# Kernel tuning notes

Hardware: AMD Instinct MI355X
Metric: run time of the kernel (lower is better)

Reference implementation:

```python
import jax, jax.numpy as jnp
import numpy as np

SIGMA = 45.0
N, M, D = 4096, 4096, 1024


def setup_inputs() -> dict:
    key = jax.random.key(0)
    k1, k2 = jax.random.split(key)
    inputs = jax.random.normal(k1, (N, D), dtype=jnp.float32)
    samples = jax.random.normal(k2, (M, D), dtype=jnp.float32)
    return {"inputs": inputs, "samples": samples}


def _sq_dists(x, y):
    # ||x_i||^2 + ||y_j||^2 - 2 x_i.y_j  -> [N, M]
    prod = x @ y.T
    xs = jnp.sum(x * x, axis=1)[:, None]
    ys = jnp.sum(y * y, axis=1)[None, :]
    return xs + ys - 2.0 * prod


def reference(inputs, samples):
    n = inputs.shape[0]
    m = samples.shape[0]
    x = inputs.reshape(n, -1)
    y = samples.reshape(m, -1)
    inv_s2 = 1.0 / (SIGMA ** 2)

    k_xx = _sq_dists(x, x)
    k_yy = _sq_dists(y, y)
    k_xy = _sq_dists(x, y)

    # unbiased MMD: exclude diagonal terms of k_xx, k_yy
    exx = jnp.exp(-k_xx * inv_s2)
    eyy = jnp.exp(-k_yy * inv_s2)
    exy = jnp.exp(-k_xy * inv_s2)

    mmd = (jnp.sum(exx) - jnp.sum(jnp.exp(-jnp.diag(k_xx) * inv_s2))) / (n * (n - 1))
    mmd = mmd + (jnp.sum(eyy) - jnp.sum(jnp.exp(-jnp.diag(k_yy) * inv_s2))) / (m * (m - 1))
    mmd = mmd - 2.0 / (n * m) * jnp.sum(exy)
    return mmd
```

## Files before the change

kernel.cpp:

```cpp
#include <hip/hip_runtime.h>
#include <math.h>


typedef _Float16 f16_t;
typedef _Float16 f16x4 __attribute__((ext_vector_type(4)));
typedef _Float16 f16x8 __attribute__((ext_vector_type(8)));
typedef float floatx4 __attribute__((ext_vector_type(4)));

#define NROWS 4096
#define MROWS 4096
#define DDIM  1024
#define BM    128
#define BK    32
#define TILE  (BM * BK)
#define NKT   (DDIM / BK)
#define PSTRIDE (4096 * BK)
#define NT    (NROWS / BM)
#define TRI   (NT * (NT + 1) / 2)
#define NBLK  (2 * TRI + NT * NT)

__global__ __launch_bounds__(256) void convert_kernel(
    const float* __restrict__ X, const float* __restrict__ Y,
    f16_t* __restrict__ Xp, f16_t* __restrict__ Yp,
    float* __restrict__ nx, float* __restrict__ ny) {
    const int wid  = threadIdx.x >> 6;
    const int lane = threadIdx.x & 63;
    const int row  = blockIdx.x * 4 + wid;
    const float* src;
    f16_t* dstp;
    float* nrm;
    int r;
    if (row < NROWS) {
        r = row;         src = X + (size_t)r * DDIM;
        dstp = Xp;  nrm = nx;
    } else {
        r = row - NROWS; src = Y + (size_t)r * DDIM;
        dstp = Yp;  nrm = ny;
    }
    const float4* s4 = (const float4*)src;
    float s = 0.f;
    #pragma unroll
    for (int c = 0; c < 4; c++) {
        float4 v = s4[c * 64 + lane];
        f16x4 h;
        h[0] = (f16_t)v.x; h[1] = (f16_t)v.y;
        h[2] = (f16_t)v.z; h[3] = (f16_t)v.w;
        *(f16x4*)(dstp + (size_t)(c * 8 + (lane >> 3)) * PSTRIDE
                       + (size_t)r * BK + (lane & 7) * 4) = h;
        float h0 = (float)h[0], h1 = (float)h[1];
        float h2 = (float)h[2], h3 = (float)h[3];
        s += h0 * h0 + h1 * h1 + h2 * h2 + h3 * h3;
    }
    #pragma unroll
    for (int off = 32; off > 0; off >>= 1) s += __shfl_down(s, off);
    if (lane == 0) nrm[r] = s;
}

__global__ __launch_bounds__(256) void mmd_mfma(
    const f16_t* __restrict__ Xp, const f16_t* __restrict__ Yp,
    const float* __restrict__ nx, const float* __restrict__ ny,
    double* __restrict__ partials) {
    __shared__ __align__(16) f16_t ldsA[TILE];
    __shared__ double wred[4];

    const int b = blockIdx.x;
    const f16_t *Ap, *Bp;
    const float *nA, *nB;
    int tr, tc;
    double coef;
    if (b < 2 * TRI) {
        int u = (b < TRI) ? b : b - TRI;
        int r = 0;
        while (u >= NT - r) { u -= NT - r; r++; }
        tr = r; tc = r + u;
        double w = (tr == tc) ? 1.0 : 2.0;
        if (b < TRI) { Ap = Xp; Bp = Xp; nA = nx; nB = nx;
                       coef = w / ((double)NROWS * (double)(NROWS - 1)); }
        else         { Ap = Yp; Bp = Yp; nA = ny; nB = ny;
                       coef = w / ((double)MROWS * (double)(MROWS - 1)); }
    } else {
        int u = b - 2 * TRI;
        tr = u >> 5; tc = u & 31;
        Ap = Xp; Bp = Yp; nA = nx; nB = ny;
        coef = -2.0 / ((double)NROWS * (double)MROWS);
    }

    const int t    = threadIdx.x;
    const int wave = t >> 6;
    const int lane = t & 63;
    const int wm   = wave >> 1;
    const int wn   = wave & 1;

    const int lr = lane >> 2;
    const int lc = (lane & 3) ^ ((lane >> 3) & 3);
    const f16_t* gsrc[2];
    f16_t* ldst[2];
    #pragma unroll
    for (int i = 0; i < 2; i++) {
        int rg = wave * 2 + i;
        gsrc[i] = Ap + (size_t)(tr * BM + rg * 16 + lr) * BK + lc * 8;
        ldst[i] = ldsA + rg * 16 * BK;
    }

    const int m    = lane & 15;
    const int quad = lane >> 4;
    const int sw8  = (quad ^ ((m >> 1) & 3)) * 8;

    const f16_t* gB = Bp + (size_t)(tc * BM + wn * 64 + m) * BK + quad * 8;

    float na[16], nb[4];
    #pragma unroll
    for (int i = 0; i < 4; i++) {
        #pragma unroll
        for (int r = 0; r < 4; r++)
            na[i * 4 + r] = nA[tr * BM + wm * 64 + i * 16 + quad * 4 + r];
        nb[i] = nB[tc * BM + wn * 64 + i * 16 + m];
    }

    floatx4 acc_r[4][4];
    #pragma unroll
    for (int i = 0; i < 4; i++)
        #pragma unroll
        for (int j = 0; j < 4; j++) acc_r[i][j] = (floatx4){0.f, 0.f, 0.f, 0.f};

    for (int kt = 0; kt < NKT; kt++) {
        const size_t ko = (size_t)kt * PSTRIDE;
        __syncthreads();
        #pragma unroll
        for (int i = 0; i < 2; i++) {
            __builtin_amdgcn_global_load_lds(
                (const __attribute__((address_space(1))) void*)(gsrc[i] + ko),
                (__attribute__((address_space(3))) void*)ldst[i],
                16, 0, 0);
        }
        __syncthreads();

        f16x8 bh[4];
        #pragma unroll
        for (int s = 0; s < 4; s++)
            bh[s] = *(const f16x8*)(gB + ko + s * 16 * BK);
        f16x8 ah[4];
        #pragma unroll
        for (int s = 0; s < 4; s++)
            ah[s] = *(const f16x8*)&ldsA[(wm * 64 + s * 16 + m) * BK + sw8];
        #pragma unroll
        for (int i = 0; i < 4; i++)
            #pragma unroll
            for (int j = 0; j < 4; j++)
                acc_r[i][j] = __builtin_amdgcn_mfma_f32_16x16x32_f16(ah[i], bh[j], acc_r[i][j], 0, 0, 0);
    }

    const float inv_s2 = 1.0f / 2025.0f;
    float lsum = 0.f;
    #pragma unroll
    for (int i = 0; i < 4; i++)
        #pragma unroll
        for (int j = 0; j < 4; j++)
            #pragma unroll
            for (int r = 0; r < 4; r++) {
                float arg = (2.f * acc_r[i][j][r] - na[i * 4 + r] - nb[j]) * inv_s2;
                lsum += __expf(arg);
            }

    double d = (double)lsum;
    #pragma unroll
    for (int off = 32; off > 0; off >>= 1) d += __shfl_down(d, off);
    if (lane == 0) wred[wave] = d;
    __syncthreads();
    if (t == 0)
        partials[b] = (wred[0] + wred[1] + wred[2] + wred[3]) * coef;
}

__global__ __launch_bounds__(256) void final_reduce(const double* __restrict__ partials,
                                                    float* __restrict__ out) {
    __shared__ double red[256];
    int t = threadIdx.x;
    double s = 0.0;
    for (int i = t; i < NBLK; i += 256) s += partials[i];
    red[t] = s;
    __syncthreads();
    for (int off = 128; off > 0; off >>= 1) {
        if (t < off) red[t] += red[t + off];
        __syncthreads();
    }
    if (t == 0) {
        double mmd = red[0] - 1.0 / (double)(NROWS - 1) - 1.0 / (double)(MROWS - 1);
        out[0] = (float)mmd;
    }
}

extern "C" void kernel_launch(void* const* d_in, const int* in_sizes, int n_in,
                              void* d_out, int out_size, void* d_ws, size_t ws_size,
                              hipStream_t stream) {
    const float* X = (const float*)d_in[0];
    const float* Y = (const float*)d_in[1];
    float* out = (float*)d_out;

    char* p = (char*)d_ws;
    double* partials = (double*)p;            p += ((size_t)NBLK * sizeof(double) + 255) & ~255ULL;
    float* nx = (float*)p;                    p += (size_t)NROWS * sizeof(float);
    float* ny = (float*)p;                    p += (size_t)MROWS * sizeof(float);
    f16_t* Xp = (f16_t*)p;                    p += (size_t)NROWS * DDIM * sizeof(f16_t);
    f16_t* Yp = (f16_t*)p;

    convert_kernel<<<(NROWS + MROWS) / 4, 256, 0, stream>>>(X, Y, Xp, Yp, nx, ny);
    mmd_mfma<<<NBLK, 256, 0, stream>>>(Xp, Yp, nx, ny, partials);
    final_reduce<<<1, 256, 0, stream>>>(partials, out);
}
```

Measured before the change: 179.1 us.

## Use 256x256 tiles with triple-buffered LDS staging of both operands

The MFMA kernel moves from 128x128 tiles with 4 waves to 256x256 tiles with 8 waves. Both the A and B operands are now staged into LDS through a 3-slot ring of async global_load_lds copies issued two k-steps ahead, with s_setprio around the MFMA block. This replaces the old scheme of one A buffer synchronized twice per step plus B read straight from global memory. The aim is to hide load latency and raise arithmetic intensity, at the cost of far fewer blocks (528 vs 2080), which may leave CUs underfilled or unbalanced, and of higher register and LDS pressure.

```diff
diff --git a/kernel.cpp b/kernel.cpp
--- a/kernel.cpp
+++ b/kernel.cpp
@@ -10,14 +10,14 @@
 #define NROWS 4096
 #define MROWS 4096
 #define DDIM  1024
-#define BM    128
 #define BK    32
-#define TILE  (BM * BK)
 #define NKT   (DDIM / BK)
 #define PSTRIDE (4096 * BK)
-#define NT    (NROWS / BM)
-#define TRI   (NT * (NT + 1) / 2)
-#define NBLK  (2 * TRI + NT * NT)
+#define BM2   256
+#define NT2   (NROWS / BM2)
+#define TRI2  (NT2 * (NT2 + 1) / 2)
+#define NBLK  (2 * TRI2 + NT2 * NT2)
+#define TSLOT (BM2 * BK)
 
 __global__ __launch_bounds__(256) void convert_kernel(
     const float* __restrict__ X, const float* __restrict__ Y,
@@ -56,119 +56,136 @@
     if (lane == 0) nrm[r] = s;
 }
 
-__global__ __launch_bounds__(256) void mmd_mfma(
+#define STAGE4(tile_, slot_) do {                                              \
+    const size_t ko_ = (size_t)(tile_) * PSTRIDE;                              \
+    _Pragma("unroll")                                                          \
+    for (int i_ = 0; i_ < 2; i_++) {                                           \
+        __builtin_amdgcn_global_load_lds(                                      \
+            (const __attribute__((address_space(1))) void*)(gA[i_] + ko_),     \
+            (__attribute__((address_space(3))) void*)(&ldsA[slot_][offAB[i_]]),\
+            16, 0, 0);                                                         \
+        __builtin_amdgcn_global_load_lds(                                      \
+            (const __attribute__((address_space(1))) void*)(gB[i_] + ko_),     \
+            (__attribute__((address_space(3))) void*)(&ldsB[slot_][offAB[i_]]),\
+            16, 0, 0);                                                         \
+    }                                                                          \
+  } while (0)
+
+__global__ __launch_bounds__(512, 2) void mmd_mfma(
     const f16_t* __restrict__ Xp, const f16_t* __restrict__ Yp,
     const float* __restrict__ nx, const float* __restrict__ ny,
     double* __restrict__ partials) {
-    __shared__ __align__(16) f16_t ldsA[TILE];
-    __shared__ double wred[4];
+    __shared__ __align__(16) f16_t ldsA[3][TSLOT];
+    __shared__ __align__(16) f16_t ldsB[3][TSLOT];
+    __shared__ double wred[8];
 
     const int b = blockIdx.x;
     const f16_t *Ap, *Bp;
     const float *nA, *nB;
     int tr, tc;
     double coef;
-    if (b < 2 * TRI) {
-        int u = (b < TRI) ? b : b - TRI;
+    if (b < 2 * TRI2) {
+        int u = (b < TRI2) ? b : b - TRI2;
         int r = 0;
-        while (u >= NT - r) { u -= NT - r; r++; }
+        while (u >= NT2 - r) { u -= NT2 - r; r++; }
         tr = r; tc = r + u;
         double w = (tr == tc) ? 1.0 : 2.0;
-        if (b < TRI) { Ap = Xp; Bp = Xp; nA = nx; nB = nx;
-                       coef = w / ((double)NROWS * (double)(NROWS - 1)); }
-        else         { Ap = Yp; Bp = Yp; nA = ny; nB = ny;
-                       coef = w / ((double)MROWS * (double)(MROWS - 1)); }
+        if (b < TRI2) { Ap = Xp; Bp = Xp; nA = nx; nB = nx;
+                        coef = w / ((double)NROWS * (double)(NROWS - 1)); }
+        else          { Ap = Yp; Bp = Yp; nA = ny; nB = ny;
+                        coef = w / ((double)MROWS * (double)(MROWS - 1)); }
     } else {
-        int u = b - 2 * TRI;
-        tr = u >> 5; tc = u & 31;
+        int u = b - 2 * TRI2;
+        tr = u >> 4; tc = u & 15;
         Ap = Xp; Bp = Yp; nA = nx; nB = ny;
         coef = -2.0 / ((double)NROWS * (double)MROWS);
     }
-
-    const int t    = threadIdx.x;
-    const int wave = t >> 6;
-    const int lane = t & 63;
-    const int wm   = wave >> 1;
-    const int wn   = wave & 1;
-
-    const int lr = lane >> 2;
-    const int lc = (lane & 3) ^ ((lane >> 3) & 3);
-    const f16_t* gsrc[2];
-    f16_t* ldst[2];
-    #pragma unroll
-    for (int i = 0; i < 2; i++) {
-        int rg = wave * 2 + i;
-        gsrc[i] = Ap + (size_t)(tr * BM + rg * 16 + lr) * BK + lc * 8;
-        ldst[i] = ldsA + rg * 16 * BK;
-    }
-
+    const int arow0 = tr * BM2, brow0 = tc * BM2;
+
+    const int tid  = threadIdx.x;
+    const int wave = tid >> 6;
+    const int lane = tid & 63;
+    const int wm   = wave >> 2;
+    const int wn   = wave & 3;
     const int m    = lane & 15;
     const int quad = lane >> 4;
     const int sw8  = (quad ^ ((m >> 1) & 3)) * 8;
 
-    const f16_t* gB = Bp + (size_t)(tc * BM + wn * 64 + m) * BK + quad * 8;
-
-    float na[16], nb[4];
-    #pragma unroll
-    for (int i = 0; i < 4; i++) {
-        #pragma unroll
-        for (int r = 0; r < 4; r++)
-            na[i * 4 + r] = nA[tr * BM + wm * 64 + i * 16 + quad * 4 + r];
-        nb[i] = nB[tc * BM + wn * 64 + i * 16 + m];
-    }
-
-    floatx4 acc_r[4][4];
-    #pragma unroll
-    for (int i = 0; i < 4; i++)
-        #pragma unroll
-        for (int j = 0; j < 4; j++) acc_r[i][j] = (floatx4){0.f, 0.f, 0.f, 0.f};
-
-    for (int kt = 0; kt < NKT; kt++) {
-        const size_t ko = (size_t)kt * PSTRIDE;
-        __syncthreads();
-        #pragma unroll
-        for (int i = 0; i < 2; i++) {
-            __builtin_amdgcn_global_load_lds(
-                (const __attribute__((address_space(1))) void*)(gsrc[i] + ko),
-                (__attribute__((address_space(3))) void*)ldst[i],
-                16, 0, 0);
-        }
-        __syncthreads();
-
-        f16x8 bh[4];
+    const int lr = lane >> 2;
+    const int lc = (lane & 3) ^ ((lane >> 3) & 3);
+    const f16_t* gA[2];
+    const f16_t* gB[2];
+    int offAB[2];
+    #pragma unroll
+    for (int i = 0; i < 2; i++) {
+        int rg = wave * 2 + i;
+        gA[i] = Ap + (size_t)(arow0 + rg * 16 + lr) * BK + lc * 8;
+        gB[i] = Bp + (size_t)(brow0 + rg * 16 + lr) * BK + lc * 8;
+        offAB[i] = rg * 16 * BK;
+    }
+
+    floatx4 acc[8][4];
+    #pragma unroll
+    for (int i = 0; i < 8; i++)
+        #pragma unroll
+        for (int j = 0; j < 4; j++) acc[i][j] = (floatx4){0.f, 0.f, 0.f, 0.f};
+
+    STAGE4(0, 0);
+    STAGE4(1, 1);
+    asm volatile("s_waitcnt vmcnt(4)" ::: "memory");
+    __builtin_amdgcn_s_barrier();
+
+    for (int t = 0; t < NKT; ++t) {
+        const int rsl = t % 3;
+        const int ssl = (t + 2) % 3;
+        const int st  = (t + 2 < NKT) ? t + 2 : NKT - 1;
+        STAGE4(st, ssl);
+        f16x8 ah[8], bh[4];
+        #pragma unroll
+        for (int s = 0; s < 8; s++)
+            ah[s] = *(const f16x8*)&ldsA[rsl][(wm * 128 + s * 16 + m) * BK + sw8];
         #pragma unroll
         for (int s = 0; s < 4; s++)
-            bh[s] = *(const f16x8*)(gB + ko + s * 16 * BK);
-        f16x8 ah[4];
-        #pragma unroll
-        for (int s = 0; s < 4; s++)
-            ah[s] = *(const f16x8*)&ldsA[(wm * 64 + s * 16 + m) * BK + sw8];
-        #pragma unroll
-        for (int i = 0; i < 4; i++)
+            bh[s] = *(const f16x8*)&ldsB[rsl][(wn * 64 + s * 16 + m) * BK + sw8];
+        __builtin_amdgcn_s_setprio(1);
+        #pragma unroll
+        for (int i = 0; i < 8; i++)
             #pragma unroll
             for (int j = 0; j < 4; j++)
-                acc_r[i][j] = __builtin_amdgcn_mfma_f32_16x16x32_f16(ah[i], bh[j], acc_r[i][j], 0, 0, 0);
+                acc[i][j] = __builtin_amdgcn_mfma_f32_16x16x32_f16(ah[i], bh[j], acc[i][j], 0, 0, 0);
+        __builtin_amdgcn_s_setprio(0);
+        asm volatile("s_waitcnt vmcnt(4)" ::: "memory");
+        __builtin_amdgcn_s_barrier();
     }
 
     const float inv_s2 = 1.0f / 2025.0f;
+    float nbv[4];
+    #pragma unroll
+    for (int j = 0; j < 4; j++) nbv[j] = nB[brow0 + wn * 64 + j * 16 + m];
     float lsum = 0.f;
     #pragma unroll
-    for (int i = 0; i < 4; i++)
+    for (int i = 0; i < 8; i++) {
+        float4 na4 = *(const float4*)&nA[arow0 + wm * 128 + i * 16 + quad * 4];
         #pragma unroll
         for (int j = 0; j < 4; j++)
             #pragma unroll
             for (int r = 0; r < 4; r++) {
-                float arg = (2.f * acc_r[i][j][r] - na[i * 4 + r] - nb[j]) * inv_s2;
+                float arg = (2.f * acc[i][j][r] - (&na4.x)[r] - nbv[j]) * inv_s2;
                 lsum += __expf(arg);
             }
+    }
 
     double d = (double)lsum;
     #pragma unroll
     for (int off = 32; off > 0; off >>= 1) d += __shfl_down(d, off);
     if (lane == 0) wred[wave] = d;
     __syncthreads();
-    if (t == 0)
-        partials[b] = (wred[0] + wred[1] + wred[2] + wred[3]) * coef;
+    if (tid == 0) {
+        double s = 0.0;
+        #pragma unroll
+        for (int w = 0; w < 8; w++) s += wred[w];
+        partials[b] = s * coef;
+    }
 }
 
 __global__ __launch_bounds__(256) void final_reduce(const double* __restrict__ partials,
@@ -204,6 +221,6 @@
     f16_t* Yp = (f16_t*)p;
 
     convert_kernel<<<(NROWS + MROWS) / 4, 256, 0, stream>>>(X, Y, Xp, Yp, nx, ny);
-    mmd_mfma<<<NBLK, 256, 0, stream>>>(Xp, Yp, nx, ny, partials);
+    mmd_mfma<<<NBLK, 512, 0, stream>>>(Xp, Yp, nx, ny, partials);
     final_reduce<<<1, 256, 0, stream>>>(partials, out);
 }
```

New measurement: 192.7 us. 1.08x slower.
